# Kernel tuning notes

Hardware: AMD Instinct MI355X
Metric: run time of the kernel (lower is better)

Reference implementation:

```python
import jax, jax.numpy as jnp
import numpy as np

B, S, E, D, H = 32, 4096, 512, 512, 512


def setup_inputs() -> dict:
    key = jax.random.key(0)
    ks = jax.random.split(key, 7)
    scale = 1.0 / np.sqrt(H)
    return {
        "encoder_hiddens": jax.random.normal(ks[0], (B, S, E), dtype=jnp.float32),
        "decoder_hidden": jax.random.normal(ks[1], (B, D), dtype=jnp.float32),
        "W_enc": jax.random.uniform(ks[2], (H, E), jnp.float32, -scale, scale),
        "b_enc": jax.random.uniform(ks[3], (H,), jnp.float32, -scale, scale),
        "W_dec": jax.random.uniform(ks[4], (H, D), jnp.float32, -scale, scale),
        "b_dec": jax.random.uniform(ks[5], (H,), jnp.float32, -scale, scale),
        "v": jax.random.uniform(ks[6], (H,), jnp.float32, -scale, scale),
    }


def reference(encoder_hiddens, decoder_hidden, W_enc, b_enc, W_dec, b_dec, v):
    # Projections (the two small GEMMs of the original per-timestep loop, batched)
    enc_hs = jnp.einsum("bse,he->bsh", encoder_hiddens, W_enc) + b_enc  # [B,S,H]
    dec_h = decoder_hidden @ W_dec.T + b_dec                            # [B,H]

    # Ragged-length detection: the torch loop breaks at the first all-zero
    # projected encoder row; positions at/after that are excluded (cumulative AND).
    nonzero = jnp.any(enc_hs != 0, axis=-1)                             # [B,S]
    valid = jnp.cumprod(nonzero.astype(jnp.int32), axis=1).astype(bool)

    # Additive (Bahdanau) scores: v . tanh(enc_hs + dec_h)
    scores = jnp.einsum("h,bsh->bs", v, jnp.tanh(enc_hs + dec_h[:, None, :]))
    scores = jnp.where(valid, scores, -jnp.inf)
    attn = jax.nn.softmax(scores, axis=1)                               # [B,S]
    attn = jnp.where(valid, attn, 0.0)

    # Weighted sum of encoder states -> context vector [B,1,E]
    return jnp.sum(encoder_hiddens * attn[..., None], axis=1, keepdims=True)
```

## Files before the change

### kernel.cpp

```cpp
#include <hip/hip_runtime.h>
#include <hip/hip_bf16.h>

#define BATCH 32
#define SEQ   4096
#define EDIM  512
#define HDIM  512

typedef unsigned short u16;
typedef unsigned int   u32;

typedef __bf16 bf16x8 __attribute__((ext_vector_type(8)));
typedef float  f32x4  __attribute__((ext_vector_type(4)));

__device__ __forceinline__ u16 bf_rne(float x) {
    u32 u = __float_as_uint(x);
    u32 r = (u + 0x7fffu + ((u >> 16) & 1u)) >> 16;
    return (u16)r;
}
__device__ __forceinline__ u32 pack2(u16 lo, u16 hi) {
    return (u32)lo | ((u32)hi << 16);
}
__device__ __forceinline__ float tanh_fast(float x) {
    float e = __builtin_amdgcn_exp2f(x * 2.88539008177793f);
    return 1.0f - 2.0f * __builtin_amdgcn_rcpf(e + 1.0f);
}

__global__ void pack_w(const float* __restrict__ W, uint4* __restrict__ out) {
    int id   = blockIdx.x * 256 + threadIdx.x;
    int nsub = id >> 10;
    int rem  = id & 1023;
    int kc   = rem >> 6;
    int lane = rem & 63;
    int row  = nsub * 16 + (lane & 15);
    int col  = kc * 32 + (lane >> 4) * 8;
    const float* src = W + row * EDIM + col;
    uint4 o;
    o.x = pack2(bf_rne(src[0]), bf_rne(src[1]));
    o.y = pack2(bf_rne(src[2]), bf_rne(src[3]));
    o.z = pack2(bf_rne(src[4]), bf_rne(src[5]));
    o.w = pack2(bf_rne(src[6]), bf_rne(src[7]));
    out[id] = o;
}

__global__ void dec_proj(const float* __restrict__ dec, const float* __restrict__ Wd,
                         const float* __restrict__ b_enc, const float* __restrict__ b_dec,
                         float* __restrict__ out) {
    int wave = threadIdx.x >> 6, lane = threadIdx.x & 63;
    int p = blockIdx.x * 4 + wave;
    int b = p >> 9, h = p & 511;
    const float4* wr = reinterpret_cast<const float4*>(Wd)  + h * 128;
    const float4* dr = reinterpret_cast<const float4*>(dec) + b * 128;
    float4 w0 = wr[lane * 2], w1 = wr[lane * 2 + 1];
    float4 d0 = dr[lane * 2], d1 = dr[lane * 2 + 1];
    float s = w0.x * d0.x + w0.y * d0.y + w0.z * d0.z + w0.w * d0.w
            + w1.x * d1.x + w1.y * d1.y + w1.z * d1.z + w1.w * d1.w;
#pragma unroll
    for (int m = 1; m < 64; m <<= 1) s += __shfl_xor(s, m, 64);
    if (lane == 0) out[p] = s + b_dec[h] + b_enc[h];
}

__global__ __launch_bounds__(256, 2) void score_kernel(
    const float* __restrict__ X, const uint4* __restrict__ Wp,
    const float* __restrict__ bias, const float* __restrict__ v,
    float* __restrict__ scores)
{
    __shared__ alignas(16) u16 Abuf[64 * 40];
    __shared__ float sred[4][64];

    const int tid  = threadIdx.x;
    const int wave = tid >> 6, lane = tid & 63;
    const int quad = lane >> 4, l15 = lane & 15;
    const int blk  = blockIdx.x;
    const long row0 = (long)blk * 64;
    const int b = blk >> 6;
    const float* Xb = X + row0 * EDIM;
    const float4* X4 = reinterpret_cast<const float4*>(Xb);

    float hb[8], hv[8];
#pragma unroll
    for (int jj = 0; jj < 8; jj++) {
        int h = wave * 128 + jj * 16 + l15;
        hb[jj] = bias[b * HDIM + h];
        hv[jj] = v[h];
    }

    f32x4 acc[4][8] = {};
    float s_acc[16];
#pragma unroll
    for (int i = 0; i < 16; i++) s_acc[i] = 0.f;

    const int r0 = tid >> 3;
    const int c0 = tid & 7;
    const int r1 = r0 + 32;

    float4 pa = X4[r0 * 128 + c0];
    float4 pb = X4[r1 * 128 + c0];

    for (int ch = 0; ch < 16; ch++) {
        __syncthreads();
        {
            u32 lo0 = pack2(bf_rne(pa.x), bf_rne(pa.y));
            u32 hi0 = pack2(bf_rne(pa.z), bf_rne(pa.w));
            u32 lo1 = pack2(bf_rne(pb.x), bf_rne(pb.y));
            u32 hi1 = pack2(bf_rne(pb.z), bf_rne(pb.w));
            uint2 s0 = make_uint2(lo0, hi0), s1 = make_uint2(lo1, hi1);
            *reinterpret_cast<uint2*>(&Abuf[r0 * 40 + c0 * 4]) = s0;
            *reinterpret_cast<uint2*>(&Abuf[r1 * 40 + c0 * 4]) = s1;
        }
        __syncthreads();
        if (ch < 15) {
            int k4 = (ch + 1) * 8;
            pa = X4[r0 * 128 + k4 + c0];
            pb = X4[r1 * 128 + k4 + c0];
        }
        bf16x8 af[4];
#pragma unroll
        for (int i = 0; i < 4; i++)
            af[i] = *reinterpret_cast<const bf16x8*>(&Abuf[(i * 16 + l15) * 40 + quad * 8]);
#pragma unroll
        for (int jj = 0; jj < 8; jj++) {
            int nsg = wave * 8 + jj;
            uint4 braw = Wp[(nsg * 16 + ch) * 64 + lane];
            bf16x8 bfr = __builtin_bit_cast(bf16x8, braw);
#pragma unroll
            for (int i = 0; i < 4; i++)
                acc[i][jj] = __builtin_amdgcn_mfma_f32_16x16x32_bf16(
                    af[i], bfr, acc[i][jj], 0, 0, 0);
        }
    }

#pragma unroll
    for (int i = 0; i < 4; i++)
#pragma unroll
        for (int jj = 0; jj < 8; jj++)
#pragma unroll
            for (int r = 0; r < 4; r++) {
                float val = acc[i][jj][r] + hb[jj];
                s_acc[i * 4 + r] += hv[jj] * tanh_fast(val);
            }

#pragma unroll
    for (int m = 1; m < 16; m <<= 1)
#pragma unroll
        for (int x = 0; x < 16; x++)
            s_acc[x] += __shfl_xor(s_acc[x], m, 16);

    if (l15 == 0) {
#pragma unroll
        for (int x = 0; x < 16; x++) {
            int i = x >> 2, r = x & 3;
            int m = i * 16 + quad * 4 + r;
            sred[wave][m] = s_acc[x];
        }
    }
    __syncthreads();
    if (tid < 64) {
        float sc = sred[0][tid] + sred[1][tid] + sred[2][tid] + sred[3][tid];
        scores[row0 + tid] = sc;
    }
}

__global__ void softmax_k(const float* __restrict__ scores, float* __restrict__ attn) {
    __shared__ float redmax[4], redsum[4];
    int b = blockIdx.x, t = threadIdx.x;
    int wave = t >> 6, lane = t & 63;
    const float* sb = scores + b * SEQ;
    float vals[16];
    float mx = -1e30f;
#pragma unroll
    for (int i = 0; i < 16; i++) { vals[i] = sb[i * 256 + t]; mx = fmaxf(mx, vals[i]); }
#pragma unroll
    for (int m = 1; m < 64; m <<= 1) mx = fmaxf(mx, __shfl_xor(mx, m, 64));
    if (lane == 0) redmax[wave] = mx;
    __syncthreads();
    mx = fmaxf(fmaxf(redmax[0], redmax[1]), fmaxf(redmax[2], redmax[3]));
    float s = 0.f;
#pragma unroll
    for (int i = 0; i < 16; i++) {
        float e = __builtin_amdgcn_exp2f((vals[i] - mx) * 1.44269504088896f);
        vals[i] = e; s += e;
    }
#pragma unroll
    for (int m = 1; m < 64; m <<= 1) s += __shfl_xor(s, m, 64);
    if (lane == 0) redsum[wave] = s;
    __syncthreads();
    s = redsum[0] + redsum[1] + redsum[2] + redsum[3];
    float inv = 1.0f / s;
    float* ab = attn + b * SEQ;
#pragma unroll
    for (int i = 0; i < 16; i++) ab[i * 256 + t] = vals[i] * inv;
}

__global__ __launch_bounds__(256) void context_k(const float* __restrict__ X,
                                                 const float* __restrict__ attn,
                                                 float* __restrict__ out) {
    __shared__ float aw[256];
    int blk = blockIdx.x;
    int b = blk >> 4, s0 = (blk & 15) << 8;
    int t = threadIdx.x;
    aw[t] = attn[b * SEQ + s0 + t];
    __syncthreads();
    const float2* Xp = reinterpret_cast<const float2*>(X) + ((long)(b * SEQ + s0)) * 256 + t;
    float ax = 0.f, ay = 0.f;
#pragma unroll 4
    for (int s = 0; s < 256; s++) {
        float w = aw[s];
        float2 x = Xp[(long)s * 256];
        ax = fmaf(w, x.x, ax);
        ay = fmaf(w, x.y, ay);
    }
    atomicAdd(&out[b * EDIM + t * 2],     ax);
    atomicAdd(&out[b * EDIM + t * 2 + 1], ay);
}

extern "C" void kernel_launch(void* const* d_in, const int* in_sizes, int n_in,
                              void* d_out, int out_size, void* d_ws, size_t ws_size,
                              hipStream_t stream) {
    const float* X      = (const float*)d_in[0];
    const float* dec    = (const float*)d_in[1];
    const float* W_enc  = (const float*)d_in[2];
    const float* b_enc  = (const float*)d_in[3];
    const float* W_dec  = (const float*)d_in[4];
    const float* b_dec  = (const float*)d_in[5];
    const float* v      = (const float*)d_in[6];
    float* out = (float*)d_out;

    char* ws = (char*)d_ws;
    uint4* wpack    = (uint4*)ws;
    float* dec_bias = (float*)(ws + (512 << 10));
    float* scores   = (float*)(ws + (512 << 10) + (64 << 10));
    float* attn     = (float*)(ws + (1024 << 10) + (64 << 10));

    hipMemsetAsync(d_out, 0, 32 * EDIM * sizeof(float), stream);

    pack_w   <<<128,  256, 0, stream>>>(W_enc, wpack);
    dec_proj <<<4096, 256, 0, stream>>>(dec, W_dec, b_enc, b_dec, dec_bias);
    score_kernel<<<2048, 256, 0, stream>>>(X, wpack, dec_bias, v, scores);
    softmax_k<<<32,   256, 0, stream>>>(scores, attn);
    context_k<<<512,  256, 0, stream>>>(X, attn, out);
}
```

Baseline: 517.6 us.

## Double-buffer score kernel LDS tiles and split context reduction across more blocks

The score kernel now double-buffers the bf16 A tile in shared memory. This drops one barrier per K-chunk and prefetches two chunks ahead, with all eight weight fragments loaded up front before the MFMAs. The context kernel splits each batch's sequence into 64-row slices over four times as many blocks, with batched loads and dual accumulators to raise memory parallelism. The cost is more atomics on the output, extra registers, and double the LDS use in the score kernel.

```diff
diff --git a/kernel.cpp b/kernel.cpp
--- a/kernel.cpp
+++ b/kernel.cpp
@@ -64,7 +64,7 @@
     const float* __restrict__ bias, const float* __restrict__ v,
     float* __restrict__ scores)
 {
-    __shared__ alignas(16) u16 Abuf[64 * 40];
+    __shared__ alignas(16) u16 Abuf[2][64 * 40];
     __shared__ float sred[4][64];
 
     const int tid  = threadIdx.x;
@@ -73,8 +73,7 @@
     const int blk  = blockIdx.x;
     const long row0 = (long)blk * 64;
     const int b = blk >> 6;
-    const float* Xb = X + row0 * EDIM;
-    const float4* X4 = reinterpret_cast<const float4*>(Xb);
+    const float4* X4 = reinterpret_cast<const float4*>(X + row0 * EDIM);
 
     float hb[8], hv[8];
 #pragma unroll
@@ -95,38 +94,51 @@
 
     float4 pa = X4[r0 * 128 + c0];
     float4 pb = X4[r1 * 128 + c0];
-
+    {
+        uint2 s0 = make_uint2(pack2(bf_rne(pa.x), bf_rne(pa.y)),
+                              pack2(bf_rne(pa.z), bf_rne(pa.w)));
+        uint2 s1 = make_uint2(pack2(bf_rne(pb.x), bf_rne(pb.y)),
+                              pack2(bf_rne(pb.z), bf_rne(pb.w)));
+        *reinterpret_cast<uint2*>(&Abuf[0][r0 * 40 + c0 * 4]) = s0;
+        *reinterpret_cast<uint2*>(&Abuf[0][r1 * 40 + c0 * 4]) = s1;
+    }
+    pa = X4[r0 * 128 + 8 + c0];
+    pb = X4[r1 * 128 + 8 + c0];
+    __syncthreads();
+
+#pragma unroll
     for (int ch = 0; ch < 16; ch++) {
-        __syncthreads();
-        {
-            u32 lo0 = pack2(bf_rne(pa.x), bf_rne(pa.y));
-            u32 hi0 = pack2(bf_rne(pa.z), bf_rne(pa.w));
-            u32 lo1 = pack2(bf_rne(pb.x), bf_rne(pb.y));
-            u32 hi1 = pack2(bf_rne(pb.z), bf_rne(pb.w));
-            uint2 s0 = make_uint2(lo0, hi0), s1 = make_uint2(lo1, hi1);
-            *reinterpret_cast<uint2*>(&Abuf[r0 * 40 + c0 * 4]) = s0;
-            *reinterpret_cast<uint2*>(&Abuf[r1 * 40 + c0 * 4]) = s1;
-        }
-        __syncthreads();
+        const int c = ch & 1;
         if (ch < 15) {
-            int k4 = (ch + 1) * 8;
+            uint2 s0 = make_uint2(pack2(bf_rne(pa.x), bf_rne(pa.y)),
+                                  pack2(bf_rne(pa.z), bf_rne(pa.w)));
+            uint2 s1 = make_uint2(pack2(bf_rne(pb.x), bf_rne(pb.y)),
+                                  pack2(bf_rne(pb.z), bf_rne(pb.w)));
+            *reinterpret_cast<uint2*>(&Abuf[c ^ 1][r0 * 40 + c0 * 4]) = s0;
+            *reinterpret_cast<uint2*>(&Abuf[c ^ 1][r1 * 40 + c0 * 4]) = s1;
+        }
+        if (ch < 14) {
+            int k4 = (ch + 2) * 8;
             pa = X4[r0 * 128 + k4 + c0];
             pb = X4[r1 * 128 + k4 + c0];
         }
+        uint4 braw[8];
+#pragma unroll
+        for (int jj = 0; jj < 8; jj++)
+            braw[jj] = Wp[((wave * 8 + jj) * 16 + ch) * 64 + lane];
         bf16x8 af[4];
 #pragma unroll
         for (int i = 0; i < 4; i++)
-            af[i] = *reinterpret_cast<const bf16x8*>(&Abuf[(i * 16 + l15) * 40 + quad * 8]);
+            af[i] = *reinterpret_cast<const bf16x8*>(&Abuf[c][(i * 16 + l15) * 40 + quad * 8]);
 #pragma unroll
         for (int jj = 0; jj < 8; jj++) {
-            int nsg = wave * 8 + jj;
-            uint4 braw = Wp[(nsg * 16 + ch) * 64 + lane];
-            bf16x8 bfr = __builtin_bit_cast(bf16x8, braw);
+            bf16x8 bfr = __builtin_bit_cast(bf16x8, braw[jj]);
 #pragma unroll
             for (int i = 0; i < 4; i++)
                 acc[i][jj] = __builtin_amdgcn_mfma_f32_16x16x32_bf16(
                     af[i], bfr, acc[i][jj], 0, 0, 0);
         }
+        __syncthreads();
     }
 
 #pragma unroll
@@ -149,14 +161,12 @@
 #pragma unroll
         for (int x = 0; x < 16; x++) {
             int i = x >> 2, r = x & 3;
-            int m = i * 16 + quad * 4 + r;
-            sred[wave][m] = s_acc[x];
+            sred[wave][i * 16 + quad * 4 + r] = s_acc[x];
         }
     }
     __syncthreads();
     if (tid < 64) {
-        float sc = sred[0][tid] + sred[1][tid] + sred[2][tid] + sred[3][tid];
-        scores[row0 + tid] = sc;
+        scores[row0 + tid] = sred[0][tid] + sred[1][tid] + sred[2][tid] + sred[3][tid];
     }
 }
 
@@ -194,23 +204,30 @@
 __global__ __launch_bounds__(256) void context_k(const float* __restrict__ X,
                                                  const float* __restrict__ attn,
                                                  float* __restrict__ out) {
-    __shared__ float aw[256];
+    __shared__ float aw[64];
     int blk = blockIdx.x;
-    int b = blk >> 4, s0 = (blk & 15) << 8;
+    int b = blk >> 6, s0 = (blk & 63) << 6;
     int t = threadIdx.x;
-    aw[t] = attn[b * SEQ + s0 + t];
+    if (t < 64) aw[t] = attn[b * SEQ + s0 + t];
     __syncthreads();
     const float2* Xp = reinterpret_cast<const float2*>(X) + ((long)(b * SEQ + s0)) * 256 + t;
-    float ax = 0.f, ay = 0.f;
+    float ax0 = 0.f, ay0 = 0.f, ax1 = 0.f, ay1 = 0.f;
 #pragma unroll 4
-    for (int s = 0; s < 256; s++) {
-        float w = aw[s];
-        float2 x = Xp[(long)s * 256];
-        ax = fmaf(w, x.x, ax);
-        ay = fmaf(w, x.y, ay);
-    }
-    atomicAdd(&out[b * EDIM + t * 2],     ax);
-    atomicAdd(&out[b * EDIM + t * 2 + 1], ay);
+    for (int s = 0; s < 64; s += 8) {
+        float2 x[8];
+#pragma unroll
+        for (int k = 0; k < 8; k++) x[k] = Xp[(long)(s + k) * 256];
+#pragma unroll
+        for (int k = 0; k < 8; k += 2) {
+            float w0 = aw[s + k], w1 = aw[s + k + 1];
+            ax0 = fmaf(w0, x[k].x,     ax0);
+            ay0 = fmaf(w0, x[k].y,     ay0);
+            ax1 = fmaf(w1, x[k + 1].x, ax1);
+            ay1 = fmaf(w1, x[k + 1].y, ay1);
+        }
+    }
+    atomicAdd(&out[b * EDIM + t * 2],     ax0 + ax1);
+    atomicAdd(&out[b * EDIM + t * 2 + 1], ay0 + ay1);
 }
 
 extern "C" void kernel_launch(void* const* d_in, const int* in_sizes, int n_in,
@@ -237,5 +254,5 @@
     dec_proj <<<4096, 256, 0, stream>>>(dec, W_dec, b_enc, b_dec, dec_bias);
     score_kernel<<<2048, 256, 0, stream>>>(X, wpack, dec_bias, v, scores);
     softmax_k<<<32,   256, 0, stream>>>(scores, attn);
-    context_k<<<512,  256, 0, stream>>>(X, attn, out);
-}
+    context_k<<<2048, 256, 0, stream>>>(X, attn, out);
+}
```

New measurement: 478.5 us. 7.5% less time.
